# Kernel tuning notes

Hardware: AMD Instinct MI355X
Metric: run time of the kernel (lower is better)

Reference implementation:

```python
import jax, jax.numpy as jnp
import numpy as np

B, F, O, DEG = 8192, 512, 512, 15  # degree+1 = 16 basis terms


def setup_inputs() -> dict:
    key = jax.random.key(0)
    k1, k2, k3 = jax.random.split(key, 3)
    x = jax.random.normal(k1, (B, F), dtype=jnp.float32)
    coeffs = jax.random.normal(k2, (F, O, DEG + 1), dtype=jnp.float32) * 0.05
    base_weight = jax.random.normal(k3, (F, O), dtype=jnp.float32) * 0.05
    return {"x": x, "coeffs": coeffs, "base_weight": base_weight}


def _chebyshev_basis(x, degree):
    # x: [B, F] -> basis: [B, F, degree+1], vectorized across all features.
    t = jnp.tanh(x)
    T0 = jnp.ones_like(t)
    T1 = t
    basis = [T0, T1]
    for _ in range(2, degree + 1):
        basis.append(2.0 * t * basis[-1] - basis[-2])
    return jnp.stack(basis, axis=-1)  # [B, F, D+1]


def reference(x, coeffs, base_weight):
    basis = _chebyshev_basis(x, DEG)                      # [B, F, D+1]
    poly_out = jnp.einsum('bin,ion->bo', basis, coeffs)   # [B, O]
    kl = jnp.zeros((1,), dtype=x.dtype)
    residual = x @ base_weight                            # [B, O]
    return (poly_out + residual, kl)
```

## Files before the change

kernel.cpp:

```cpp
#include <hip/hip_runtime.h>
#include <hip/hip_bf16.h>
#include <stdint.h>

#define MB_ 8192
#define FD  512
#define OD  512
#define KD  8704
#define KBASIS 8192
#define BT_KS   1088
#define BT_CHUNKS_PER_CT (BT_KS * 128)
#define BT_BYTES_PER_CT  (BT_CHUNKS_PER_CT * 16)
#define TOFF 65536
#define WS_T    16777216ull
#define WS_XBF  8388608ull

typedef __attribute__((ext_vector_type(4))) float f32x4;
typedef __attribute__((ext_vector_type(8))) short bf16x8;
typedef __attribute__((ext_vector_type(4))) unsigned int u32x4;
typedef __attribute__((ext_vector_type(2))) unsigned int u32x2;

__device__ __forceinline__ void gload_lds16(const void* g, void* l) {
  __builtin_amdgcn_global_load_lds((const __attribute__((address_space(1))) void*)g,
                                   (__attribute__((address_space(3))) void*)l,
                                   16, 0, 0);
}

__device__ __forceinline__ uint32_t bf_rtn(float f) {
  uint32_t u = __float_as_uint(f);
  return (u + 0x7fffu + ((u >> 16) & 1u)) >> 16;
}

__device__ __forceinline__ uint32_t pk(float a, float b) {
  uint32_t r;
  asm("v_cvt_pk_bf16_f32 %0, %1, %2" : "=v"(r) : "v"(a), "v"(b));
  return r;
}

__global__ __launch_bounds__(256) void k_prep(const float* __restrict__ x,
                                              float* __restrict__ t,
                                              uint16_t* __restrict__ xbf,
                                              const float* __restrict__ coeffs,
                                              const float* __restrict__ bw,
                                              uint16_t* __restrict__ bt2) {
  if (blockIdx.x < 4096) {
    int i = blockIdx.x * 256 + threadIdx.x;
    f32x4 v = ((const f32x4*)x)[i];
    f32x4 tv;
    tv[0] = tanhf(v[0]); tv[1] = tanhf(v[1]);
    tv[2] = tanhf(v[2]); tv[3] = tanhf(v[3]);
    ((f32x4*)t)[i] = tv;
    u32x2 p;
    p[0] = pk(v[0], v[1]);
    p[1] = pk(v[2], v[3]);
    ((u32x2*)xbf)[i] = p;
  } else {
    int tid = (blockIdx.x - 4096) * 256 + threadIdx.x;
    {
      int o = tid & 511, i = tid >> 9;
      const f32x4* src = (const f32x4*)(coeffs + (((size_t)(i * 512 + o)) << 4));
      f32x4 c0 = src[0], c1 = src[1], c2 = src[2], c3 = src[3];
      u32x4 qa, qb;
      qa[0] = pk(c0[0], c0[1]);
      qa[1] = pk(c0[2], c0[3]);
      qa[2] = pk(c1[0], c1[1]);
      qa[3] = pk(c1[2], c1[3]);
      qb[0] = pk(c2[0], c2[1]);
      qb[1] = pk(c2[2], c2[3]);
      qb[2] = pk(c3[0], c3[1]);
      qb[3] = pk(c3[2], c3[3]);
      int slo = ((i >> 2) << 3) | (i & 3);
      size_t cidx = (size_t)(o >> 7) * BT_CHUNKS_PER_CT + (size_t)slo * 128 + (o & 127);
      u32x4* base = (u32x4*)bt2;
      base[cidx]       = qa;
      base[cidx + 512] = qb;
    }
    {
      int o2 = tid >> 9, i2 = tid & 511;
      size_t cidx = (size_t)(o2 >> 7) * BT_CHUNKS_PER_CT + (size_t)(1024 + (i2 >> 3)) * 128 + (o2 & 127);
      bt2[cidx * 8 + (i2 & 7)] = (uint16_t)bf_rtn(bw[i2 * 512 + o2]);
    }
  }
}

template <int MODE>
__device__ __forceinline__ void gemm_body(int bx, char* lds,
                                          const float* __restrict__ t,
                                          const uint16_t* __restrict__ xbf,
                                          const uint16_t* __restrict__ bt2,
                                          float* __restrict__ outp) {
  constexpr int S0 = (MODE == 2) ? 68 : 0;

  const int tid  = threadIdx.x;
  const int lane = tid & 63;
  const int wid  = tid >> 6;
  const int wr   = wid >> 1;
  const int wc   = wid & 1;
  const int l15  = lane & 15, l4 = lane >> 4;

  int idx = bx >> 3;
  int rt  = (bx & 7) * 8 + (idx >> 2);
  int ct  = idx & 3;
  const int brow = rt << 7, bcol = ct << 7;

  const char* btbase = (const char*)bt2 + (size_t)ct * BT_BYTES_PER_CT;
  const int row = brow + wr * 32 + l15;
  const uint16_t* x0 = xbf + (size_t)row * FD;
  const uint16_t* x1 = x0 + (size_t)16 * FD;

  const char* bb0 = lds + l4 * 2048 + (wc * 64 + l15) * 16;
  const char* tb0 = lds + TOFF + (wr * 32 + l15) * 16 + l4 * 4;
  char* sBl = lds + tid * 16;
  char* sTl = lds + TOFF + wid * 1024 + lane * 16;

  const char* sBgBase = btbase + (size_t)tid * 16;
  const char* sTgBase = (const char*)t + (((size_t)(brow + wid * 64 + lane)) * FD) * 4;

  f32x4 acc[2][4];
#pragma unroll
  for (int m = 0; m < 2; ++m)
#pragma unroll
    for (int n = 0; n < 4; ++n) acc[m][n] = (f32x4)0.0f;

  u32x4 pf00 = {}, pf01 = {}, pf10 = {}, pf11 = {};

  auto stageB = [&](int gs, int b2) {
    const char* src = sBgBase + ((size_t)gs << 14);
    gload_lds16(src, sBl + b2 * 16384);
    gload_lds16(src + 8192, sBl + b2 * 16384 + 8192);
  };
  auto stageT = [&](int gs, int b2) {
    if (wid < 2)
      gload_lds16(sTgBase + ((size_t)gs << 4), sTl + b2 * 2048);
  };
  auto chains = [&](const char* tb, u32x4& af00, u32x4& af01,
                    u32x4& af10, u32x4& af11) {
#pragma unroll
    for (int m = 0; m < 2; ++m) {
      float tv = *(const float*)(tb + m * 256);
      float c2 = tv + tv;
      float T0 = 1.0f, T1 = tv;
      float T2  = __builtin_fmaf(c2, T1,  -T0);
      float T3  = __builtin_fmaf(c2, T2,  -T1);
      float T4  = __builtin_fmaf(c2, T3,  -T2);
      float T5  = __builtin_fmaf(c2, T4,  -T3);
      float T6  = __builtin_fmaf(c2, T5,  -T4);
      float T7  = __builtin_fmaf(c2, T6,  -T5);
      float T8  = __builtin_fmaf(c2, T7,  -T6);
      float T9  = __builtin_fmaf(c2, T8,  -T7);
      float T10 = __builtin_fmaf(c2, T9,  -T8);
      float T11 = __builtin_fmaf(c2, T10, -T9);
      float T12 = __builtin_fmaf(c2, T11, -T10);
      float T13 = __builtin_fmaf(c2, T12, -T11);
      float T14 = __builtin_fmaf(c2, T13, -T12);
      float T15 = __builtin_fmaf(c2, T14, -T13);
      u32x4 lo, hi;
      lo[0] = pk(T0,  T1);  lo[1] = pk(T2,  T3);
      lo[2] = pk(T4,  T5);  lo[3] = pk(T6,  T7);
      hi[0] = pk(T8,  T9);  hi[1] = pk(T10, T11);
      hi[2] = pk(T12, T13); hi[3] = pk(T14, T15);
      if (m == 0) { af00 = lo; af01 = hi; }
      else        { af10 = lo; af11 = hi; }
    }
  };
  auto mfma16 = [&](const char* bb, const u32x4& af00, const u32x4& af01,
                    const u32x4& af10, const u32x4& af11) {
    bf16x8 a00 = *(const bf16x8*)&af00;
    bf16x8 a01 = *(const bf16x8*)&af01;
    bf16x8 a10 = *(const bf16x8*)&af10;
    bf16x8 a11 = *(const bf16x8*)&af11;
#pragma unroll
    for (int n = 0; n < 4; ++n) {
      bf16x8 b0 = *(const bf16x8*)(bb + n * 256);
      bf16x8 b1 = *(const bf16x8*)(bb + 8192 + n * 256);
      acc[0][n] = __builtin_amdgcn_mfma_f32_16x16x32_bf16(a00, b0, acc[0][n], 0, 0, 0);
      acc[1][n] = __builtin_amdgcn_mfma_f32_16x16x32_bf16(a10, b0, acc[1][n], 0, 0, 0);
      acc[0][n] = __builtin_amdgcn_mfma_f32_16x16x32_bf16(a01, b1, acc[0][n], 0, 0, 0);
      acc[1][n] = __builtin_amdgcn_mfma_f32_16x16x32_bf16(a11, b1, acc[1][n], 0, 0, 0);
    }
  };
  auto fence_bar = [&]() {
    if (wid < 2) asm volatile("s_waitcnt vmcnt(6)" ::: "memory");
    else         asm volatile("s_waitcnt vmcnt(4)" ::: "memory");
    __builtin_amdgcn_s_barrier();
    __builtin_amdgcn_sched_barrier(0);
  };
  auto pairbody = [&](int s, int c0, int c1) {
    u32x4 af00, af01, af10, af11;
    chains(tb0 + c0 * 2048, af00, af01, af10, af11);
    __builtin_amdgcn_s_setprio(1);
    mfma16(bb0 + c0 * 16384, af00, af01, af10, af11);
    __builtin_amdgcn_s_setprio(0);
    chains(tb0 + c1 * 2048, af00, af01, af10, af11);
    __builtin_amdgcn_s_setprio(1);
    mfma16(bb0 + c1 * 16384, af00, af01, af10, af11);
    __builtin_amdgcn_s_setprio(0);
    __builtin_amdgcn_s_barrier();
    __builtin_amdgcn_sched_barrier(0);
    stageB(S0 + s + 4, c0); stageT(S0 + s + 4, c0);
    stageB(S0 + s + 5, c1); stageT(S0 + s + 5, c1);
    fence_bar();
  };

  stageB(S0 + 0, 0); stageT(S0 + 0, 0);
  stageB(S0 + 1, 1); stageT(S0 + 1, 1);
  stageB(S0 + 2, 2); stageT(S0 + 2, 2);
  stageB(S0 + 3, 3); stageT(S0 + 3, 3);
  fence_bar();

  if constexpr (MODE == 1) {
    for (int s = 0; s < 64; s += 4) { pairbody(s, 0, 1); pairbody(s + 2, 2, 3); }
    for (int s = 64; s < 68; ++s) {
      u32x4 af00, af01, af10, af11;
      chains(tb0 + (s & 3) * 2048, af00, af01, af10, af11);
      mfma16(bb0 + (s & 3) * 16384, af00, af01, af10, af11);
      __syncthreads();
    }
  } else {
    for (int s = 0; s < 56; s += 4) { pairbody(s, 0, 1); pairbody(s + 2, 2, 3); }
    for (int s = 56; s < 68; ++s) {
      u32x4 af00 = pf00, af01 = pf01, af10 = pf10, af11 = pf11;
      if (s >= 58 && s <= 65) stageB(68 + s + 2, (s + 2) & 3);
      if (s >= 59 && s <= 66) {
        int kres = ((s + 1 - 60) << 6) + l4 * 8;
        pf00 = *(const u32x4*)(x0 + kres);
        pf01 = *(const u32x4*)(x0 + kres + 32);
        pf10 = *(const u32x4*)(x1 + kres);
        pf11 = *(const u32x4*)(x1 + kres + 32);
      }
      if (s < 60) chains(tb0 + (s & 3) * 2048, af00, af01, af10, af11);
      mfma16(bb0 + (s & 3) * 16384, af00, af01, af10, af11);
      __syncthreads();
    }
  }

#pragma unroll
  for (int m = 0; m < 2; ++m)
#pragma unroll
    for (int n = 0; n < 4; ++n)
#pragma unroll
      for (int r = 0; r < 4; ++r) {
        int grow = brow + wr * 32 + m * 16 + l4 * 4 + r;
        int gcol = bcol + wc * 64 + n * 16 + l15;
        __hip_atomic_fetch_add(&outp[(size_t)grow * OD + gcol], acc[m][n][r],
                               __ATOMIC_RELAXED, __HIP_MEMORY_SCOPE_AGENT);
      }
}

__global__ __launch_bounds__(512, 4) void k_gemm_split(const float* __restrict__ t,
                                                       const uint16_t* __restrict__ xbf,
                                                       const uint16_t* __restrict__ bt2,
                                                       float* __restrict__ out) {
  __shared__ __align__(128) char lds[73728];
  if (blockIdx.x < 256) gemm_body<1>(blockIdx.x,       lds, t, xbf, bt2, out);
  else                  gemm_body<2>(blockIdx.x - 256, lds, t, xbf, bt2, out);
}

extern "C" void kernel_launch(void* const* d_in, const int* in_sizes, int n_in,
                              void* d_out, int out_size, void* d_ws, size_t ws_size,
                              hipStream_t stream) {
  const float* x      = (const float*)d_in[0];
  const float* coeffs = (const float*)d_in[1];
  const float* bw     = (const float*)d_in[2];
  float* out = (float*)d_out;
  char* ws = (char*)d_ws;

  float*    t   = (float*)ws;
  uint16_t* xbf = (uint16_t*)(ws + WS_T);
  uint16_t* bt2 = (uint16_t*)(ws + WS_T + WS_XBF);

  hipMemsetAsync(d_out, 0, (size_t)out_size * sizeof(float), stream);
  k_prep<<<5120, 256, 0, stream>>>(x, t, xbf, coeffs, bw, bt2);
  k_gemm_split<<<512, 512, 0, stream>>>(t, xbf, bt2, out);
}
```

Measured before the change: 117.1 us.

## Replace split-K atomics and memset with plain stores plus bf16 partial reduction pass

Removes the output memset and per-element atomic adds for the two K-split halves. The first half now stores its results directly to the output, and the second half writes a bf16 partial buffer in workspace, which a new elementwise kernel adds into the output. The kl scalar zeroing moves into the prep kernel. This trades atomic traffic and the memset for an extra launch and an extra read/write pass. Rounding the second partial to bf16 also costs some precision.

```diff
diff --git a/kernel.cpp b/kernel.cpp
--- a/kernel.cpp
+++ b/kernel.cpp
@@ -13,6 +13,8 @@
 #define TOFF 65536
 #define WS_T    16777216ull
 #define WS_XBF  8388608ull
+#define WS_BT2  8912896ull
+#define WS_P1_OFF (WS_T + WS_XBF + WS_BT2)
 
 typedef __attribute__((ext_vector_type(4))) float f32x4;
 typedef __attribute__((ext_vector_type(8))) short bf16x8;
@@ -41,7 +43,8 @@
                                               uint16_t* __restrict__ xbf,
                                               const float* __restrict__ coeffs,
                                               const float* __restrict__ bw,
-                                              uint16_t* __restrict__ bt2) {
+                                              uint16_t* __restrict__ bt2,
+                                              float* __restrict__ out) {
   if (blockIdx.x < 4096) {
     int i = blockIdx.x * 256 + threadIdx.x;
     f32x4 v = ((const f32x4*)x)[i];
@@ -79,6 +82,7 @@
       size_t cidx = (size_t)(o2 >> 7) * BT_CHUNKS_PER_CT + (size_t)(1024 + (i2 >> 3)) * 128 + (o2 & 127);
       bt2[cidx * 8 + (i2 & 7)] = (uint16_t)bf_rtn(bw[i2 * 512 + o2]);
     }
+    if (tid == 0) out[(size_t)MB_ * OD] = 0.0f;
   }
 }
 
@@ -87,7 +91,8 @@
                                           const float* __restrict__ t,
                                           const uint16_t* __restrict__ xbf,
                                           const uint16_t* __restrict__ bt2,
-                                          float* __restrict__ outp) {
+                                          float* __restrict__ outp,
+                                          uint16_t* __restrict__ p1b) {
   constexpr int S0 = (MODE == 2) ? 68 : 0;
 
   const int tid  = threadIdx.x;
@@ -241,18 +246,33 @@
       for (int r = 0; r < 4; ++r) {
         int grow = brow + wr * 32 + m * 16 + l4 * 4 + r;
         int gcol = bcol + wc * 64 + n * 16 + l15;
-        __hip_atomic_fetch_add(&outp[(size_t)grow * OD + gcol], acc[m][n][r],
-                               __ATOMIC_RELAXED, __HIP_MEMORY_SCOPE_AGENT);
+        if constexpr (MODE == 1)
+          outp[(size_t)grow * OD + gcol] = acc[m][n][r];
+        else
+          p1b[(size_t)grow * OD + gcol] = (uint16_t)bf_rtn(acc[m][n][r]);
       }
 }
 
 __global__ __launch_bounds__(512, 4) void k_gemm_split(const float* __restrict__ t,
                                                        const uint16_t* __restrict__ xbf,
                                                        const uint16_t* __restrict__ bt2,
-                                                       float* __restrict__ out) {
+                                                       float* __restrict__ out,
+                                                       uint16_t* __restrict__ p1b) {
   __shared__ __align__(128) char lds[73728];
-  if (blockIdx.x < 256) gemm_body<1>(blockIdx.x,       lds, t, xbf, bt2, out);
-  else                  gemm_body<2>(blockIdx.x - 256, lds, t, xbf, bt2, out);
+  if (blockIdx.x < 256) gemm_body<1>(blockIdx.x,       lds, t, xbf, bt2, out, p1b);
+  else                  gemm_body<2>(blockIdx.x - 256, lds, t, xbf, bt2, out, p1b);
+}
+
+__global__ __launch_bounds__(256) void k_add(float* __restrict__ out,
+                                             const uint16_t* __restrict__ p1b) {
+  size_t i = ((size_t)blockIdx.x * 256 + threadIdx.x) * 4;
+  f32x4 a = *(const f32x4*)(out + i);
+  u32x2 p = *(const u32x2*)(p1b + i);
+  a[0] += __uint_as_float(p[0] << 16);
+  a[1] += __uint_as_float(p[0] & 0xffff0000u);
+  a[2] += __uint_as_float(p[1] << 16);
+  a[3] += __uint_as_float(p[1] & 0xffff0000u);
+  *(f32x4*)(out + i) = a;
 }
 
 extern "C" void kernel_launch(void* const* d_in, const int* in_sizes, int n_in,
@@ -267,8 +287,9 @@
   float*    t   = (float*)ws;
   uint16_t* xbf = (uint16_t*)(ws + WS_T);
   uint16_t* bt2 = (uint16_t*)(ws + WS_T + WS_XBF);
-
-  hipMemsetAsync(d_out, 0, (size_t)out_size * sizeof(float), stream);
-  k_prep<<<5120, 256, 0, stream>>>(x, t, xbf, coeffs, bw, bt2);
-  k_gemm_split<<<512, 512, 0, stream>>>(t, xbf, bt2, out);
-}
+  uint16_t* p1b = (uint16_t*)(ws + WS_P1_OFF);
+
+  k_prep<<<5120, 256, 0, stream>>>(x, t, xbf, coeffs, bw, bt2, out);
+  k_gemm_split<<<512, 512, 0, stream>>>(t, xbf, bt2, out, p1b);
+  k_add<<<4096, 256, 0, stream>>>(out, p1b);
+}
```

Measured after the change: 102.2 us. -12.7%, faster.
